# Performance work log

Hardware: AMD Instinct MI355X
Metric: run time of the kernel (lower is better)

The kernel has to match this reference:

```python
import jax, jax.numpy as jnp
import numpy as np

B, S, H = 4, 2048, 768
NUM_POS = B * (S // 4)  # fixed count of positive clc_label entries (2048, even)
NEG_BIG = -1000000000.0


def setup_inputs() -> dict:
    key = jax.random.key(0)
    k1, k2, k3, k4, k5 = jax.random.split(key, 5)
    encoded_states = jax.random.normal(k1, (B, S, H), dtype=jnp.float32)
    # sorted cell-ids -> contiguous segments for the equality mask
    indicator = jnp.sort(jax.random.randint(k2, (B, S), 0, 256, dtype=jnp.int32), axis=-1)
    # clc_label: first S//4 positions per row are positive targets (class ids in [1,S)),
    # last S//2 positions are -1 (attendable keys), rest 0 (ignored)
    pos_labels = jax.random.randint(k3, (B, S // 4), 1, S, dtype=jnp.int32)
    clc_label = jnp.zeros((B, S), dtype=jnp.int32)
    clc_label = clc_label.at[:, : S // 4].set(pos_labels)
    clc_label = clc_label.at[:, S // 2:].set(-1)
    # uniform_linear params (torch Linear: y = x @ W.T + b)
    W = jax.random.normal(k4, (H, H), dtype=jnp.float32) / np.sqrt(H)
    b = jax.random.normal(k5, (H,), dtype=jnp.float32) * 0.01
    return {"encoded_states": encoded_states, "W": W, "b": b,
            "indicator": indicator, "clc_label": clc_label}


def _ce(logits, labels):
    # mean cross entropy; all labels are > 0 here so ignore_index=0 never triggers
    logp = jax.nn.log_softmax(logits, axis=-1)
    return -jnp.take_along_axis(logp, labels[:, None], axis=1).mean()


def reference(encoded_states, W, b, indicator, clc_label):
    # indicator-equality mask matmul == within-segment sum (the segment-reduce emulation)
    seg_mask = (indicator[:, :, None] == indicator[:, None, :]).astype(encoded_states.dtype)  # [B,S,S]
    agg = jnp.einsum("bij,bjh->bih", seg_mask, encoded_states)  # [B,S,H]
    # Q and K use the SAME linear on the same input -> compute once
    proj = jnp.tanh(agg @ W.T + b)  # [B,S,H]
    scores = jnp.einsum("bih,bjh->bij", proj, proj)  # [B,S,S]
    # attend only to positions where clc_label < 0
    allow = (clc_label < 0)[:, None, :]  # [B,1,S]
    scores = scores + jnp.where(allow, 0.0, NEG_BIG).astype(scores.dtype)
    flat = scores.reshape(-1, S)          # [B*S, S]
    labels = clc_label.reshape(-1)        # [B*S]
    pos_idx = jnp.nonzero(labels > 0, size=NUM_POS)[0]  # row-major order == torch bool-indexing
    logits = flat[pos_idx]                # [NUM_POS, S]
    labs = labels[pos_idx]                # [NUM_POS]
    sep_logits, sep_labels = logits[0::2], labs[0::2]
    tok_logits, tok_labels = logits[1::2], labs[1::2]
    sep_loss = _ce(sep_logits, sep_labels)
    tok_loss = _ce(tok_logits, tok_labels)
    sep_correct = jnp.sum((jnp.argmax(sep_logits, axis=-1).astype(jnp.int32) == sep_labels).astype(jnp.float32))
    tok_correct = jnp.sum((jnp.argmax(tok_logits, axis=-1).astype(jnp.int32) == tok_labels).astype(jnp.float32))
    sep_count = jnp.asarray(sep_logits.shape[0] + 1e-6, dtype=jnp.float32)
    tok_count = jnp.asarray(tok_logits.shape[0] + 1e-6, dtype=jnp.float32)
    return ((sep_loss, sep_correct, sep_count), (tok_loss, tok_correct, tok_count))
```

## Files before the change

### kernel.cpp

```cpp
#include <hip/hip_runtime.h>
#include <math.h>
#include <limits.h>

#define BB 4
#define SS 2048
#define HH 768
#define MAXSEG 256
#define NUM_POS (BB*(SS/4))
#define NEG_BIG -1000000000.0f

typedef _Float16 f16x8 __attribute__((ext_vector_type(8)));
typedef _Float16 f16x4 __attribute__((ext_vector_type(4)));
typedef float    f32x4 __attribute__((ext_vector_type(4)));

__global__ __launch_bounds__(256) void k_scan(
    const int* __restrict__ ind, const int* __restrict__ clc,
    int* __restrict__ seg_id, int* __restrict__ seg_start,
    int* __restrict__ nseg, int* __restrict__ pos_local, int* __restrict__ pos_cnt,
    int* __restrict__ allowCnt, int* __restrict__ firstAllow)
{
  int b = blockIdx.x, t = threadIdx.x;
  int lane = t & 63, wid = t >> 6;
  __shared__ int sInd[SS];
  __shared__ int sWave[4];
  __shared__ int sAC[MAXSEG];
  __shared__ int sFA[MAXSEG];
  for (int i = t; i < SS; i += 256) sInd[i] = ind[b*SS + i];
  sAC[t] = 0; sFA[t] = INT_MAX;
  __syncthreads();

  int i0 = t * 8;
  int f[8], cv[8];
  int lsum = 0;
  #pragma unroll
  for (int u = 0; u < 8; u++) {
    int i = i0 + u;
    f[u] = (i == 0) ? 0 : (sInd[i] != sInd[i-1]);
    cv[u] = clc[b*SS + i];
    lsum += f[u];
  }
  int x = lsum;
  #pragma unroll
  for (int off = 1; off < 64; off <<= 1) {
    int v = __shfl_up(x, off, 64);
    if (lane >= off) x += v;
  }
  if (lane == 63) sWave[wid] = x;
  __syncthreads();
  int base = 0;
  for (int w = 0; w < wid; w++) base += sWave[w];
  int run = base + x - lsum;
  int rid[8];
  #pragma unroll
  for (int u = 0; u < 8; u++) {
    int i = i0 + u;
    run += f[u];
    rid[u] = run;
    seg_id[b*SS + i] = run;
    if (f[u] || i == 0) seg_start[b*(MAXSEG+1) + run] = i;
  }
  if (t == 255) { nseg[b] = run + 1; seg_start[b*(MAXSEG+1) + run + 1] = SS; }

  #pragma unroll
  for (int u = 0; u < 8; u++) {
    if (cv[u] < 0) {
      atomicAdd(&sAC[rid[u]], 1);
      atomicMin(&sFA[rid[u]], i0 + u);
    }
  }
  __syncthreads();
  allowCnt[b*MAXSEG + t]   = sAC[t];
  firstAllow[b*MAXSEG + t] = sFA[t];

  int psum = 0;
  int p[8];
  #pragma unroll
  for (int u = 0; u < 8; u++) { p[u] = (cv[u] > 0) ? 1 : 0; psum += p[u]; }
  x = psum;
  #pragma unroll
  for (int off = 1; off < 64; off <<= 1) {
    int v = __shfl_up(x, off, 64);
    if (lane >= off) x += v;
  }
  __syncthreads();
  if (lane == 63) sWave[wid] = x;
  __syncthreads();
  base = 0;
  for (int w = 0; w < wid; w++) base += sWave[w];
  int rank = base + x - psum;
  #pragma unroll
  for (int u = 0; u < 8; u++) {
    if (p[u]) { pos_local[b*SS + rank] = i0 + u; rank++; }
  }
  if (t == 255) pos_cnt[b] = rank;
}

__global__ __launch_bounds__(256) void k_segsum(
    const float* __restrict__ es, const float* __restrict__ W,
    const int* __restrict__ seg_start, const int* __restrict__ nseg,
    _Float16* __restrict__ segsum_h, _Float16* __restrict__ Wh)
{
  int blk = blockIdx.x, t = threadIdx.x;
  if (blk >= BB*MAXSEG) {
    int idx = (blk - BB*MAXSEG)*256 + t;
    float4 v = ((const float4*)W)[idx];
    f16x4 h;
    h[0] = (_Float16)v.x; h[1] = (_Float16)v.y;
    h[2] = (_Float16)v.z; h[3] = (_Float16)v.w;
    *(f16x4*)(Wh + (size_t)idx*4) = h;
    return;
  }
  int b = blk >> 8, s = blk & 255;
  _Float16* o = segsum_h + ((size_t)b*MAXSEG + s)*HH;
  if (s >= nseg[b]) {
    o[t] = (_Float16)0.f; o[t+256] = (_Float16)0.f; o[t+512] = (_Float16)0.f;
    return;
  }
  int st = seg_start[b*(MAXSEG+1) + s];
  int en = seg_start[b*(MAXSEG+1) + s + 1];
  const float* base = es + (size_t)b*SS*HH;
  float a0 = 0.f, a1 = 0.f, a2 = 0.f;
  for (int i = st; i < en; i++) {
    const float* r = base + (size_t)i*HH;
    a0 += r[t]; a1 += r[t+256]; a2 += r[t+512];
  }
  o[t] = (_Float16)a0; o[t+256] = (_Float16)a1; o[t+512] = (_Float16)a2;
}

__global__ __launch_bounds__(256) void k_gemmU(
    const _Float16* __restrict__ Ah, const _Float16* __restrict__ Wh,
    const float* __restrict__ bias, _Float16* __restrict__ Uh)
{
  int tid = threadIdx.x;
  int w = tid >> 6, lane = tid & 63;
  int tile = blockIdx.x*4 + w;
  int tm = tile / 24, tn = tile % 24;
  int rb = tm*32, cb = tn*32;
  int m0 = lane & 15, quad = lane >> 4;
  const _Float16* A0 = Ah + (size_t)(rb + m0)*HH + quad*8;
  const _Float16* A1 = A0 + (size_t)16*HH;
  const _Float16* B0 = Wh + (size_t)(cb + m0)*HH + quad*8;
  const _Float16* B1 = B0 + (size_t)16*HH;
  f32x4 acc00 = {0.f,0.f,0.f,0.f}, acc01 = {0.f,0.f,0.f,0.f};
  f32x4 acc10 = {0.f,0.f,0.f,0.f}, acc11 = {0.f,0.f,0.f,0.f};
  #pragma unroll 4
  for (int k0 = 0; k0 < HH; k0 += 32) {
    f16x8 a0 = *(const f16x8*)(A0 + k0);
    f16x8 a1 = *(const f16x8*)(A1 + k0);
    f16x8 b0 = *(const f16x8*)(B0 + k0);
    f16x8 b1 = *(const f16x8*)(B1 + k0);
    acc00 = __builtin_amdgcn_mfma_f32_16x16x32_f16(a0, b0, acc00, 0, 0, 0);
    acc01 = __builtin_amdgcn_mfma_f32_16x16x32_f16(a0, b1, acc01, 0, 0, 0);
    acc10 = __builtin_amdgcn_mfma_f32_16x16x32_f16(a1, b0, acc10, 0, 0, 0);
    acc11 = __builtin_amdgcn_mfma_f32_16x16x32_f16(a1, b1, acc11, 0, 0, 0);
  }
  float bc0 = bias[cb + m0], bc1 = bias[cb + 16 + m0];
  int r0 = rb + quad*4;
  #pragma unroll
  for (int i = 0; i < 4; i++) {
    Uh[(size_t)(r0+i)*HH    + cb + m0]      = (_Float16)tanhf(acc00[i] + bc0);
    Uh[(size_t)(r0+i)*HH    + cb + 16 + m0] = (_Float16)tanhf(acc01[i] + bc1);
    Uh[(size_t)(r0+16+i)*HH + cb + m0]      = (_Float16)tanhf(acc10[i] + bc0);
    Uh[(size_t)(r0+16+i)*HH + cb + 16 + m0] = (_Float16)tanhf(acc11[i] + bc1);
  }
}

__global__ __launch_bounds__(256) void k_gram(
    const _Float16* __restrict__ Uh, float* __restrict__ G)
{
  int tid = threadIdx.x;
  int w = tid >> 6, lane = tid & 63;
  int tile = blockIdx.x*4 + w;
  int b = tile >> 8, rem = tile & 255;
  int rb = (rem >> 4)*16, cb = (rem & 15)*16;
  int m0 = lane & 15, quad = lane >> 4;
  const _Float16* Ub = Uh + (size_t)b*MAXSEG*HH;
  const _Float16* A0 = Ub + (size_t)(rb + m0)*HH + quad*8;
  const _Float16* B0 = Ub + (size_t)(cb + m0)*HH + quad*8;
  f32x4 acc = {0.f,0.f,0.f,0.f};
  #pragma unroll 4
  for (int k0 = 0; k0 < HH; k0 += 32) {
    f16x8 a  = *(const f16x8*)(A0 + k0);
    f16x8 bb = *(const f16x8*)(B0 + k0);
    acc = __builtin_amdgcn_mfma_f32_16x16x32_f16(a, bb, acc, 0, 0, 0);
  }
  float* Gb = G + (size_t)b*MAXSEG*MAXSEG;
  int r0 = rb + quad*4;
  #pragma unroll
  for (int i = 0; i < 4; i++)
    Gb[(size_t)(r0+i)*MAXSEG + cb + m0] = acc[i];
}

__global__ __launch_bounds__(256) void k_seglse(
    const float* __restrict__ G, const int* __restrict__ allowCnt,
    const int* __restrict__ firstAllow, const int* __restrict__ nseg,
    float* __restrict__ lse, int* __restrict__ amax)
{
  int lane = threadIdx.x & 63, wid = threadIdx.x >> 6;
  int row = blockIdx.x * 4 + wid;
  int b = row >> 8, si = row & 255;
  if (si >= nseg[b]) return;
  const float* g = G + ((size_t)b*MAXSEG + si)*MAXSEG;
  const int* ac = allowCnt + b*MAXSEG;
  const int* fa = firstAllow + b*MAXSEG;

  float gv[4]; int av[4], fv[4];
  #pragma unroll
  for (int q = 0; q < 4; q++) {
    int s = lane + 64*q;
    gv[q] = g[s]; av[q] = ac[s]; fv[q] = fa[s];
  }
  float m = -INFINITY;
  #pragma unroll
  for (int q = 0; q < 4; q++) if (av[q] > 0) m = fmaxf(m, gv[q]);
  #pragma unroll
  for (int off = 32; off > 0; off >>= 1) m = fmaxf(m, __shfl_xor(m, off, 64));
  float s = 0.f;
  #pragma unroll
  for (int q = 0; q < 4; q++) if (av[q] > 0) s += (float)av[q] * expf(gv[q] - m);
  #pragma unroll
  for (int off = 32; off > 0; off >>= 1) s += __shfl_xor(s, off, 64);
  float bv = -INFINITY; int bi = INT_MAX;
  #pragma unroll
  for (int q = 0; q < 4; q++) {
    if (av[q] > 0 && (gv[q] > bv || (gv[q] == bv && fv[q] < bi))) { bv = gv[q]; bi = fv[q]; }
  }
  #pragma unroll
  for (int off = 32; off > 0; off >>= 1) {
    float ov = __shfl_xor(bv, off, 64);
    int   oi = __shfl_xor(bi, off, 64);
    if (ov > bv || (ov == bv && oi < bi)) { bv = ov; bi = oi; }
  }
  if (lane == 0) {
    lse[row]  = m + logf(s);
    amax[row] = bi;
  }
}

__global__ __launch_bounds__(256) void k_posfinal(
    const float* __restrict__ G, const int* __restrict__ seg_id,
    const int* __restrict__ clc, const int* __restrict__ pos_local,
    const int* __restrict__ pos_cnt, const float* __restrict__ lse,
    const int* __restrict__ amax, float* __restrict__ out)
{
  __shared__ int sBase[BB+1];
  __shared__ float sL0[4], sC0[4], sL1[4], sC1[4];
  int t = threadIdx.x;
  if (t == 0) {
    int acc = 0; sBase[0] = 0;
    for (int b = 0; b < BB; b++) { acc += pos_cnt[b]; sBase[b+1] = acc; }
  }
  __syncthreads();
  int total = sBase[BB];
  if (total > NUM_POS) total = NUM_POS;
  float l0 = 0.f, c0 = 0.f, l1 = 0.f, c1 = 0.f;
  for (int r = t; r < total; r += 256) {
    int b = 0;
    while (b < BB-1 && r >= sBase[b+1]) b++;
    int k = r - sBase[b];
    int i  = pos_local[b*SS + k];
    int si = seg_id[b*SS + i];
    int L  = clc[b*SS + i];
    int sL = seg_id[b*SS + L];
    float vL = G[((size_t)b*MAXSEG + si)*MAXSEG + sL] + (clc[b*SS + L] < 0 ? 0.0f : NEG_BIG);
    float loss = lse[b*MAXSEG + si] - vL;
    float corr = (amax[b*MAXSEG + si] == L) ? 1.0f : 0.0f;
    if (r & 1) { l1 += loss; c1 += corr; } else { l0 += loss; c0 += corr; }
  }
  int lane = t & 63, wid = t >> 6;
  #pragma unroll
  for (int off = 32; off > 0; off >>= 1) {
    l0 += __shfl_down(l0, off, 64);
    c0 += __shfl_down(c0, off, 64);
    l1 += __shfl_down(l1, off, 64);
    c1 += __shfl_down(c1, off, 64);
  }
  if (lane == 0) { sL0[wid] = l0; sC0[wid] = c0; sL1[wid] = l1; sC1[wid] = c1; }
  __syncthreads();
  if (t == 0) {
    float L0 = sL0[0]+sL0[1]+sL0[2]+sL0[3];
    float C0 = sC0[0]+sC0[1]+sC0[2]+sC0[3];
    float L1 = sL1[0]+sL1[1]+sL1[2]+sL1[3];
    float C1 = sC1[0]+sC1[1]+sC1[2]+sC1[3];
    float n = (float)(NUM_POS/2);
    out[0] = L0 / n;
    out[1] = C0;
    out[2] = n + 1e-6f;
    out[3] = L1 / n;
    out[4] = C1;
    out[5] = n + 1e-6f;
  }
}

extern "C" void kernel_launch(void* const* d_in, const int* in_sizes, int n_in,
                              void* d_out, int out_size, void* d_ws, size_t ws_size,
                              hipStream_t stream)
{
  const float* es   = (const float*)d_in[0];
  const float* W    = (const float*)d_in[1];
  const float* bias = (const float*)d_in[2];
  const int*   ind  = (const int*)d_in[3];
  const int*   clc  = (const int*)d_in[4];
  float* out = (float*)d_out;

  char* ws = (char*)d_ws;
  int*   nseg       = (int*)(ws + 0);
  int*   pos_cnt    = (int*)(ws + 256);
  int*   seg_start  = (int*)(ws + 1024);
  int*   seg_id     = (int*)(ws + 8192);
  int*   pos_local  = (int*)(ws + 40960);
  int*   allowCnt   = (int*)(ws + 73728);
  int*   firstAllow = (int*)(ws + 77824);
  float* lse        = (float*)(ws + 81920);
  int*   amax       = (int*)(ws + 86016);
  _Float16* segsum_h = (_Float16*)(ws + 90112);
  _Float16* Wh       = (_Float16*)(ws + 1662976);
  _Float16* Uh       = (_Float16*)(ws + 2842624);
  float*    G        = (float*)(ws + 4415488);

  k_scan<<<BB, 256, 0, stream>>>(ind, clc, seg_id, seg_start, nseg, pos_local,
                                 pos_cnt, allowCnt, firstAllow);
  k_segsum<<<BB*MAXSEG + 576, 256, 0, stream>>>(es, W, seg_start, nseg, segsum_h, Wh);
  k_gemmU<<<192, 256, 0, stream>>>(segsum_h, Wh, bias, Uh);
  k_gram<<<256, 256, 0, stream>>>(Uh, G);
  k_seglse<<<(BB*MAXSEG)/4, 256, 0, stream>>>(G, allowCnt, firstAllow, nseg, lse, amax);
  k_posfinal<<<1, 256, 0, stream>>>(G, seg_id, clc, pos_local, pos_cnt, lse, amax, out);
}
```

Measured before the change: 124.2 us.

## Fuse segment LSE and positive-row loss into one tail kernel with atomic finish

Merges the per-segment logsumexp/argmax kernel and the single-block positive-row loss kernel into one k_tail kernel. The scan kernel now also buckets positive rows by segment and carries their global rank parity. Each tail block then reduces its own positives and combines results through global atomics and a last-block counter. The W fp16 conversion moves from k_segsum into k_scan, and k_segsum switches to float4 loads with 192 threads. This removes one launch and the serial single-block tail, at the cost of more scan work and float atomics whose summation order is nondeterministic.

After: 132.4 us. 6.6% more time.

```diff
diff --git a/kernel.cpp b/kernel.cpp
--- a/kernel.cpp
+++ b/kernel.cpp
@@ -13,96 +13,33 @@
 typedef _Float16 f16x4 __attribute__((ext_vector_type(4)));
 typedef float    f32x4 __attribute__((ext_vector_type(4)));
 
+__device__ __forceinline__ int blockExclScan(int v, int* sWave, int lane, int wid)
+{
+  int x = v;
+  #pragma unroll
+  for (int off = 1; off < 64; off <<= 1) {
+    int y = __shfl_up(x, off, 64);
+    if (lane >= off) x += y;
+  }
+  if (lane == 63) sWave[wid] = x;
+  __syncthreads();
+  int base = 0;
+  for (int w = 0; w < wid; w++) base += sWave[w];
+  return base + x - v;
+}
+
 __global__ __launch_bounds__(256) void k_scan(
     const int* __restrict__ ind, const int* __restrict__ clc,
+    const float* __restrict__ W, _Float16* __restrict__ Wh,
     int* __restrict__ seg_id, int* __restrict__ seg_start,
-    int* __restrict__ nseg, int* __restrict__ pos_local, int* __restrict__ pos_cnt,
-    int* __restrict__ allowCnt, int* __restrict__ firstAllow)
-{
-  int b = blockIdx.x, t = threadIdx.x;
-  int lane = t & 63, wid = t >> 6;
-  __shared__ int sInd[SS];
-  __shared__ int sWave[4];
-  __shared__ int sAC[MAXSEG];
-  __shared__ int sFA[MAXSEG];
-  for (int i = t; i < SS; i += 256) sInd[i] = ind[b*SS + i];
-  sAC[t] = 0; sFA[t] = INT_MAX;
-  __syncthreads();
-
-  int i0 = t * 8;
-  int f[8], cv[8];
-  int lsum = 0;
-  #pragma unroll
-  for (int u = 0; u < 8; u++) {
-    int i = i0 + u;
-    f[u] = (i == 0) ? 0 : (sInd[i] != sInd[i-1]);
-    cv[u] = clc[b*SS + i];
-    lsum += f[u];
-  }
-  int x = lsum;
-  #pragma unroll
-  for (int off = 1; off < 64; off <<= 1) {
-    int v = __shfl_up(x, off, 64);
-    if (lane >= off) x += v;
-  }
-  if (lane == 63) sWave[wid] = x;
-  __syncthreads();
-  int base = 0;
-  for (int w = 0; w < wid; w++) base += sWave[w];
-  int run = base + x - lsum;
-  int rid[8];
-  #pragma unroll
-  for (int u = 0; u < 8; u++) {
-    int i = i0 + u;
-    run += f[u];
-    rid[u] = run;
-    seg_id[b*SS + i] = run;
-    if (f[u] || i == 0) seg_start[b*(MAXSEG+1) + run] = i;
-  }
-  if (t == 255) { nseg[b] = run + 1; seg_start[b*(MAXSEG+1) + run + 1] = SS; }
-
-  #pragma unroll
-  for (int u = 0; u < 8; u++) {
-    if (cv[u] < 0) {
-      atomicAdd(&sAC[rid[u]], 1);
-      atomicMin(&sFA[rid[u]], i0 + u);
-    }
-  }
-  __syncthreads();
-  allowCnt[b*MAXSEG + t]   = sAC[t];
-  firstAllow[b*MAXSEG + t] = sFA[t];
-
-  int psum = 0;
-  int p[8];
-  #pragma unroll
-  for (int u = 0; u < 8; u++) { p[u] = (cv[u] > 0) ? 1 : 0; psum += p[u]; }
-  x = psum;
-  #pragma unroll
-  for (int off = 1; off < 64; off <<= 1) {
-    int v = __shfl_up(x, off, 64);
-    if (lane >= off) x += v;
-  }
-  __syncthreads();
-  if (lane == 63) sWave[wid] = x;
-  __syncthreads();
-  base = 0;
-  for (int w = 0; w < wid; w++) base += sWave[w];
-  int rank = base + x - psum;
-  #pragma unroll
-  for (int u = 0; u < 8; u++) {
-    if (p[u]) { pos_local[b*SS + rank] = i0 + u; rank++; }
-  }
-  if (t == 255) pos_cnt[b] = rank;
-}
-
-__global__ __launch_bounds__(256) void k_segsum(
-    const float* __restrict__ es, const float* __restrict__ W,
-    const int* __restrict__ seg_start, const int* __restrict__ nseg,
-    _Float16* __restrict__ segsum_h, _Float16* __restrict__ Wh)
-{
-  int blk = blockIdx.x, t = threadIdx.x;
-  if (blk >= BB*MAXSEG) {
-    int idx = (blk - BB*MAXSEG)*256 + t;
+    int* __restrict__ nseg, int* __restrict__ pos_cnt,
+    int* __restrict__ allowCnt, int* __restrict__ firstAllow,
+    int* __restrict__ posSegOff, int* __restrict__ posSeg,
+    float* __restrict__ accum, int* __restrict__ counter)
+{
+  int t = threadIdx.x;
+  if (blockIdx.x >= BB) {
+    int idx = (blockIdx.x - BB)*256 + t;
     float4 v = ((const float4*)W)[idx];
     f16x4 h;
     h[0] = (_Float16)v.x; h[1] = (_Float16)v.y;
@@ -110,21 +47,106 @@
     *(f16x4*)(Wh + (size_t)idx*4) = h;
     return;
   }
+  int b = blockIdx.x;
+  int lane = t & 63, wid = t >> 6;
+  __shared__ int sInd[SS];
+  __shared__ int sWave[4];
+  __shared__ int sAC[MAXSEG];
+  __shared__ int sFA[MAXSEG];
+  if (b == 0 && t < 4) accum[t] = 0.f;
+  if (b == 0 && t == 4) *counter = 0;
+  for (int i = t; i < SS; i += 256) sInd[i] = ind[b*SS + i];
+  sAC[t] = 0; sFA[t] = INT_MAX;
+  __syncthreads();
+
+  int i0 = t * 8;
+  int f[8], cv[8];
+  int lsum = 0;
+  #pragma unroll
+  for (int u = 0; u < 8; u++) {
+    int i = i0 + u;
+    f[u] = (i == 0) ? 0 : (sInd[i] != sInd[i-1]);
+    cv[u] = clc[b*SS + i];
+    lsum += f[u];
+  }
+  int run = blockExclScan(lsum, sWave, lane, wid);
+  int rid[8];
+  #pragma unroll
+  for (int u = 0; u < 8; u++) {
+    int i = i0 + u;
+    run += f[u];
+    rid[u] = run;
+    seg_id[b*SS + i] = run;
+    if (f[u] || i == 0) seg_start[b*(MAXSEG+1) + run] = i;
+  }
+  if (t == 255) { nseg[b] = run + 1; seg_start[b*(MAXSEG+1) + run + 1] = SS; }
+
+  #pragma unroll
+  for (int u = 0; u < 8; u++) {
+    if (cv[u] < 0) {
+      atomicAdd(&sAC[rid[u]], 1);
+      atomicMin(&sFA[rid[u]], i0 + u);
+    }
+  }
+  __syncthreads();
+  allowCnt[b*MAXSEG + t]   = sAC[t];
+  firstAllow[b*MAXSEG + t] = sFA[t];
+  __syncthreads();
+
+  int p[8], kk[8];
+  int psum = 0;
+  #pragma unroll
+  for (int u = 0; u < 8; u++) { p[u] = (cv[u] > 0) ? 1 : 0; psum += p[u]; }
+  int rank = blockExclScan(psum, sWave, lane, wid);
+  #pragma unroll
+  for (int u = 0; u < 8; u++) {
+    kk[u] = rank;
+    if (p[u]) rank++;
+  }
+  if (t == 255) pos_cnt[b] = rank;
+  __syncthreads();
+
+  sAC[t] = 0;
+  __syncthreads();
+  #pragma unroll
+  for (int u = 0; u < 8; u++) if (p[u]) atomicAdd(&sAC[rid[u]], 1);
+  __syncthreads();
+  int cnt = sAC[t];
+  int off = blockExclScan(cnt, sWave, lane, wid);
+  posSegOff[b*(MAXSEG+1) + t] = off;
+  if (t == 255) posSegOff[b*(MAXSEG+1) + 256] = off + cnt;
+  __syncthreads();
+  sFA[t] = off;
+  __syncthreads();
+  #pragma unroll
+  for (int u = 0; u < 8; u++) {
+    if (p[u]) {
+      int pos = atomicAdd(&sFA[rid[u]], 1);
+      posSeg[b*SS + pos] = (kk[u] << 16) | (i0 + u);
+    }
+  }
+}
+
+__global__ __launch_bounds__(192) void k_segsum(
+    const float* __restrict__ es, const int* __restrict__ seg_start,
+    const int* __restrict__ nseg, _Float16* __restrict__ segsum_h)
+{
+  int blk = blockIdx.x, t = threadIdx.x;
   int b = blk >> 8, s = blk & 255;
-  _Float16* o = segsum_h + ((size_t)b*MAXSEG + s)*HH;
-  if (s >= nseg[b]) {
-    o[t] = (_Float16)0.f; o[t+256] = (_Float16)0.f; o[t+512] = (_Float16)0.f;
-    return;
-  }
-  int st = seg_start[b*(MAXSEG+1) + s];
-  int en = seg_start[b*(MAXSEG+1) + s + 1];
-  const float* base = es + (size_t)b*SS*HH;
-  float a0 = 0.f, a1 = 0.f, a2 = 0.f;
-  for (int i = st; i < en; i++) {
-    const float* r = base + (size_t)i*HH;
-    a0 += r[t]; a1 += r[t+256]; a2 += r[t+512];
-  }
-  o[t] = (_Float16)a0; o[t+256] = (_Float16)a1; o[t+512] = (_Float16)a2;
+  float4 acc = {0.f, 0.f, 0.f, 0.f};
+  if (s < nseg[b]) {
+    int st = seg_start[b*(MAXSEG+1) + s];
+    int en = seg_start[b*(MAXSEG+1) + s + 1];
+    const float* basep = es + (size_t)b*SS*HH + t*4;
+    for (int i = st; i < en; i++) {
+      float4 v = *(const float4*)(basep + (size_t)i*HH);
+      acc.x += v.x; acc.y += v.y; acc.z += v.z; acc.w += v.w;
+    }
+  }
+  f16x4 h;
+  h[0] = (_Float16)acc.x; h[1] = (_Float16)acc.y;
+  h[2] = (_Float16)acc.z; h[3] = (_Float16)acc.w;
+  *(f16x4*)(segsum_h + ((size_t)b*MAXSEG + s)*HH + t*4) = h;
 }
 
 __global__ __launch_bounds__(256) void k_gemmU(
@@ -191,83 +213,72 @@
     Gb[(size_t)(r0+i)*MAXSEG + cb + m0] = acc[i];
 }
 
-__global__ __launch_bounds__(256) void k_seglse(
-    const float* __restrict__ G, const int* __restrict__ allowCnt,
-    const int* __restrict__ firstAllow, const int* __restrict__ nseg,
-    float* __restrict__ lse, int* __restrict__ amax)
-{
-  int lane = threadIdx.x & 63, wid = threadIdx.x >> 6;
+__global__ __launch_bounds__(256) void k_tail(
+    const float* __restrict__ G, const int* __restrict__ seg_id,
+    const int* __restrict__ clc, const int* __restrict__ nseg,
+    const int* __restrict__ pos_cnt, const int* __restrict__ allowCnt,
+    const int* __restrict__ firstAllow, const int* __restrict__ posSegOff,
+    const int* __restrict__ posSeg,
+    float* __restrict__ accum, int* __restrict__ counter,
+    float* __restrict__ out)
+{
+  __shared__ float sP[4][4];
+  int t = threadIdx.x;
+  int lane = t & 63, wid = t >> 6;
   int row = blockIdx.x * 4 + wid;
   int b = row >> 8, si = row & 255;
-  if (si >= nseg[b]) return;
-  const float* g = G + ((size_t)b*MAXSEG + si)*MAXSEG;
-  const int* ac = allowCnt + b*MAXSEG;
-  const int* fa = firstAllow + b*MAXSEG;
-
-  float gv[4]; int av[4], fv[4];
-  #pragma unroll
-  for (int q = 0; q < 4; q++) {
-    int s = lane + 64*q;
-    gv[q] = g[s]; av[q] = ac[s]; fv[q] = fa[s];
-  }
-  float m = -INFINITY;
-  #pragma unroll
-  for (int q = 0; q < 4; q++) if (av[q] > 0) m = fmaxf(m, gv[q]);
-  #pragma unroll
-  for (int off = 32; off > 0; off >>= 1) m = fmaxf(m, __shfl_xor(m, off, 64));
-  float s = 0.f;
-  #pragma unroll
-  for (int q = 0; q < 4; q++) if (av[q] > 0) s += (float)av[q] * expf(gv[q] - m);
-  #pragma unroll
-  for (int off = 32; off > 0; off >>= 1) s += __shfl_xor(s, off, 64);
-  float bv = -INFINITY; int bi = INT_MAX;
-  #pragma unroll
-  for (int q = 0; q < 4; q++) {
-    if (av[q] > 0 && (gv[q] > bv || (gv[q] == bv && fv[q] < bi))) { bv = gv[q]; bi = fv[q]; }
-  }
-  #pragma unroll
-  for (int off = 32; off > 0; off >>= 1) {
-    float ov = __shfl_xor(bv, off, 64);
-    int   oi = __shfl_xor(bi, off, 64);
-    if (ov > bv || (ov == bv && oi < bi)) { bv = ov; bi = oi; }
-  }
-  if (lane == 0) {
-    lse[row]  = m + logf(s);
-    amax[row] = bi;
-  }
-}
-
-__global__ __launch_bounds__(256) void k_posfinal(
-    const float* __restrict__ G, const int* __restrict__ seg_id,
-    const int* __restrict__ clc, const int* __restrict__ pos_local,
-    const int* __restrict__ pos_cnt, const float* __restrict__ lse,
-    const int* __restrict__ amax, float* __restrict__ out)
-{
-  __shared__ int sBase[BB+1];
-  __shared__ float sL0[4], sC0[4], sL1[4], sC1[4];
-  int t = threadIdx.x;
-  if (t == 0) {
-    int acc = 0; sBase[0] = 0;
-    for (int b = 0; b < BB; b++) { acc += pos_cnt[b]; sBase[b+1] = acc; }
-  }
-  __syncthreads();
-  int total = sBase[BB];
-  if (total > NUM_POS) total = NUM_POS;
+
   float l0 = 0.f, c0 = 0.f, l1 = 0.f, c1 = 0.f;
-  for (int r = t; r < total; r += 256) {
-    int b = 0;
-    while (b < BB-1 && r >= sBase[b+1]) b++;
-    int k = r - sBase[b];
-    int i  = pos_local[b*SS + k];
-    int si = seg_id[b*SS + i];
-    int L  = clc[b*SS + i];
-    int sL = seg_id[b*SS + L];
-    float vL = G[((size_t)b*MAXSEG + si)*MAXSEG + sL] + (clc[b*SS + L] < 0 ? 0.0f : NEG_BIG);
-    float loss = lse[b*MAXSEG + si] - vL;
-    float corr = (amax[b*MAXSEG + si] == L) ? 1.0f : 0.0f;
-    if (r & 1) { l1 += loss; c1 += corr; } else { l0 += loss; c0 += corr; }
-  }
-  int lane = t & 63, wid = t >> 6;
+  if (si < nseg[b]) {
+    const float* g = G + ((size_t)b*MAXSEG + si)*MAXSEG;
+    const int* ac = allowCnt + b*MAXSEG;
+    const int* fa = firstAllow + b*MAXSEG;
+    float gv[4]; int av[4], fv[4];
+    #pragma unroll
+    for (int q = 0; q < 4; q++) {
+      int s = lane + 64*q;
+      gv[q] = g[s]; av[q] = ac[s]; fv[q] = fa[s];
+    }
+    float m = -INFINITY;
+    #pragma unroll
+    for (int q = 0; q < 4; q++) if (av[q] > 0) m = fmaxf(m, gv[q]);
+    #pragma unroll
+    for (int off = 32; off > 0; off >>= 1) m = fmaxf(m, __shfl_xor(m, off, 64));
+    float s = 0.f;
+    #pragma unroll
+    for (int q = 0; q < 4; q++) if (av[q] > 0) s += (float)av[q] * expf(gv[q] - m);
+    #pragma unroll
+    for (int off = 32; off > 0; off >>= 1) s += __shfl_xor(s, off, 64);
+    float bv = -INFINITY; int bi = INT_MAX;
+    #pragma unroll
+    for (int q = 0; q < 4; q++) {
+      if (av[q] > 0 && (gv[q] > bv || (gv[q] == bv && fv[q] < bi))) { bv = gv[q]; bi = fv[q]; }
+    }
+    #pragma unroll
+    for (int off = 32; off > 0; off >>= 1) {
+      float ov = __shfl_xor(bv, off, 64);
+      int   oi = __shfl_xor(bi, off, 64);
+      if (ov > bv || (ov == bv && oi < bi)) { bv = ov; bi = oi; }
+    }
+    float lseV = m + logf(s);
+
+    int base_b = 0;
+    for (int bb2 = 0; bb2 < b; bb2++) base_b += pos_cnt[bb2];
+    int st = posSegOff[b*(MAXSEG+1) + si];
+    int en = posSegOff[b*(MAXSEG+1) + si + 1];
+    for (int pp = st + lane; pp < en; pp += 64) {
+      int e = posSeg[b*SS + pp];
+      int i = e & 0xFFFF, k = e >> 16;
+      int L = clc[b*SS + i];
+      int sL = seg_id[b*SS + L];
+      float vL = G[((size_t)b*MAXSEG + si)*MAXSEG + sL]
+               + (clc[b*SS + L] < 0 ? 0.0f : NEG_BIG);
+      float loss = lseV - vL;
+      float corr = (bi == L) ? 1.0f : 0.0f;
+      if ((base_b + k) & 1) { l1 += loss; c1 += corr; }
+      else                  { l0 += loss; c0 += corr; }
+    }
+  }
   #pragma unroll
   for (int off = 32; off > 0; off >>= 1) {
     l0 += __shfl_down(l0, off, 64);
@@ -275,20 +286,32 @@
     l1 += __shfl_down(l1, off, 64);
     c1 += __shfl_down(c1, off, 64);
   }
-  if (lane == 0) { sL0[wid] = l0; sC0[wid] = c0; sL1[wid] = l1; sC1[wid] = c1; }
+  if (lane == 0) { sP[wid][0] = l0; sP[wid][1] = c0; sP[wid][2] = l1; sP[wid][3] = c1; }
   __syncthreads();
   if (t == 0) {
-    float L0 = sL0[0]+sL0[1]+sL0[2]+sL0[3];
-    float C0 = sC0[0]+sC0[1]+sC0[2]+sC0[3];
-    float L1 = sL1[0]+sL1[1]+sL1[2]+sL1[3];
-    float C1 = sC1[0]+sC1[1]+sC1[2]+sC1[3];
-    float n = (float)(NUM_POS/2);
-    out[0] = L0 / n;
-    out[1] = C0;
-    out[2] = n + 1e-6f;
-    out[3] = L1 / n;
-    out[4] = C1;
-    out[5] = n + 1e-6f;
+    float v0 = sP[0][0]+sP[1][0]+sP[2][0]+sP[3][0];
+    float v1 = sP[0][1]+sP[1][1]+sP[2][1]+sP[3][1];
+    float v2 = sP[0][2]+sP[1][2]+sP[2][2]+sP[3][2];
+    float v3 = sP[0][3]+sP[1][3]+sP[2][3]+sP[3][3];
+    atomicAdd(&accum[0], v0);
+    atomicAdd(&accum[1], v1);
+    atomicAdd(&accum[2], v2);
+    atomicAdd(&accum[3], v3);
+    __threadfence();
+    int old = atomicAdd(counter, 1);
+    if (old == gridDim.x - 1) {
+      float L0 = atomicAdd(&accum[0], 0.0f);
+      float C0 = atomicAdd(&accum[1], 0.0f);
+      float L1 = atomicAdd(&accum[2], 0.0f);
+      float C1 = atomicAdd(&accum[3], 0.0f);
+      float n = (float)(NUM_POS/2);
+      out[0] = L0 / n;
+      out[1] = C0;
+      out[2] = n + 1e-6f;
+      out[3] = L1 / n;
+      out[4] = C1;
+      out[5] = n + 1e-6f;
+    }
   }
 }
 
@@ -304,25 +327,28 @@
   float* out = (float*)d_out;
 
   char* ws = (char*)d_ws;
-  int*   nseg       = (int*)(ws + 0);
-  int*   pos_cnt    = (int*)(ws + 256);
+  float* accum      = (float*)(ws + 0);
+  int*   counter    = (int*)(ws + 16);
+  int*   nseg       = (int*)(ws + 256);
+  int*   pos_cnt    = (int*)(ws + 512);
   int*   seg_start  = (int*)(ws + 1024);
   int*   seg_id     = (int*)(ws + 8192);
-  int*   pos_local  = (int*)(ws + 40960);
-  int*   allowCnt   = (int*)(ws + 73728);
-  int*   firstAllow = (int*)(ws + 77824);
-  float* lse        = (float*)(ws + 81920);
-  int*   amax       = (int*)(ws + 86016);
+  int*   posSegOff  = (int*)(ws + 40960);
+  int*   posSeg     = (int*)(ws + 49152);
+  int*   allowCnt   = (int*)(ws + 81920);
+  int*   firstAllow = (int*)(ws + 86016);
   _Float16* segsum_h = (_Float16*)(ws + 90112);
   _Float16* Wh       = (_Float16*)(ws + 1662976);
   _Float16* Uh       = (_Float16*)(ws + 2842624);
   float*    G        = (float*)(ws + 4415488);
 
-  k_scan<<<BB, 256, 0, stream>>>(ind, clc, seg_id, seg_start, nseg, pos_local,
-                                 pos_cnt, allowCnt, firstAllow);
-  k_segsum<<<BB*MAXSEG + 576, 256, 0, stream>>>(es, W, seg_start, nseg, segsum_h, Wh);
+  k_scan<<<BB + 576, 256, 0, stream>>>(ind, clc, W, Wh, seg_id, seg_start,
+                                       nseg, pos_cnt, allowCnt, firstAllow,
+                                       posSegOff, posSeg, accum, counter);
+  k_segsum<<<BB*MAXSEG, 192, 0, stream>>>(es, seg_start, nseg, segsum_h);
   k_gemmU<<<192, 256, 0, stream>>>(segsum_h, Wh, bias, Uh);
   k_gram<<<256, 256, 0, stream>>>(Uh, G);
-  k_seglse<<<(BB*MAXSEG)/4, 256, 0, stream>>>(G, allowCnt, firstAllow, nseg, lse, amax);
-  k_posfinal<<<1, 256, 0, stream>>>(G, seg_id, clc, pos_local, pos_cnt, lse, amax, out);
-}
+  k_tail<<<256, 256, 0, stream>>>(G, seg_id, clc, nseg, pos_cnt, allowCnt,
+                                  firstAllow, posSegOff, posSeg,
+                                  accum, counter, out);
+}
```
